# Performance work log

Measured on AMD Instinct MI355X. Metric: run time of the kernel, lower is better.

## Reference

```python
import jax, jax.numpy as jnp
import numpy as np

B, L, D, H, P = 4, 4096, 1024, 8, 4
DPH = D // H


def _grid_sample_row(v, grid):
    """F.grid_sample for a (N, C, 1, Lv) input, bilinear, padding_mode='zeros',
    align_corners=False. v: (N, C, Lv), grid: (N, Lq, P, 2) with (x, y) in last dim.
    Returns (N, C, Lq, P)."""
    N, C, Lv = v.shape
    x = grid[..., 0]
    y = grid[..., 1]
    # unnormalize (align_corners=False): u = ((coord + 1) * size - 1) / 2
    ux = ((x + 1.0) * Lv - 1.0) * 0.5          # width = Lv
    uy = ((y + 1.0) * 1.0 - 1.0) * 0.5         # height = 1
    x0f = jnp.floor(ux)
    wx1 = ux - x0f
    wx0 = 1.0 - wx1
    y0f = jnp.floor(uy)
    wy1 = uy - y0f
    wy0 = 1.0 - wy1
    # only row 0 exists; rows outside contribute zero (padding zeros)
    wy = wy0 * (y0f == 0.0) + wy1 * ((y0f + 1.0) == 0.0)   # (N, Lq, P)
    i0 = x0f.astype(jnp.int32)
    i1 = i0 + 1
    m0 = (i0 >= 0) & (i0 < Lv)
    m1 = (i1 >= 0) & (i1 < Lv)
    i0c = jnp.clip(i0, 0, Lv - 1)
    i1c = jnp.clip(i1, 0, Lv - 1)
    # gather along width per batch element: (C, Lv)[:, (Lq, P)] -> (C, Lq, P)
    v0 = jax.vmap(lambda vv, ii: vv[:, ii])(v, i0c)
    v1 = jax.vmap(lambda vv, ii: vv[:, ii])(v, i1c)
    w0 = (wx0 * m0 * wy)[:, None, :, :]
    w1 = (wx1 * m1 * wy)[:, None, :, :]
    return v0 * w0 + v1 * w1


def setup_inputs() -> dict:
    key = jax.random.key(0)
    ks = jax.random.split(key, 16)
    s = 0.02
    f32 = jnp.float32
    return {
        "query": jax.random.normal(ks[0], (B, L, D), f32),
        "key_in": jax.random.normal(ks[1], (B, L, D), f32),
        "value": jax.random.normal(ks[2], (B, L, D), f32),
        "Wqk": jax.random.normal(ks[3], (D, 2 * D), f32) * s,
        "bqk": jnp.zeros((2 * D,), f32),
        "Wv": jax.random.normal(ks[4], (D, D), f32) * s,
        "bv": jnp.zeros((D,), f32),
        "Woff": jax.random.normal(ks[5], (D, H * P * 2), f32) * s,
        "boff": jax.random.normal(ks[6], (H * P * 2,), f32) * 0.25,
        "Wattn": jax.random.normal(ks[7], (D, H * P), f32) * s,
        "battn": jnp.zeros((H * P,), f32),
        "Wo": jax.random.normal(ks[8], (D, D), f32) * s,
        "bo": jnp.zeros((D,), f32),
    }


def reference(query, key_in, value, Wqk, bqk, Wv, bv, Woff, boff, Wattn, battn, Wo, bo):
    # qk_proj: q, k are computed in the original but never used downstream (dead code)
    qk = query @ Wqk + bqk
    q, k = jnp.split(qk, 2, axis=-1)  # noqa: unused, matches original

    v = value @ Wv + bv                                   # (B, L, D)

    # reference points: x base = linspace[0] = 0, y base = i/(L-1) for query i
    ref_y = jnp.linspace(0.0, 1.0, L)
    ref = jnp.stack([jnp.zeros_like(ref_y), ref_y], axis=-1)   # (L, 2)

    offsets = (query @ Woff + boff).reshape(B, L, H, P, 2)
    attn = jax.nn.softmax((query @ Wattn + battn).reshape(B, L, H, P), axis=-1)

    loc = jnp.clip(ref[None, :, None, None, :] + offsets, 0.0, 1.0)  # (B, L, H, P, 2)

    # value -> (B*H, dph, L)
    vh = v.reshape(B, L, H, DPH).transpose(0, 2, 3, 1).reshape(B * H, DPH, L)
    grid = loc.transpose(0, 2, 1, 3, 4).reshape(B * H, L, P, 2)

    sampled = _grid_sample_row(vh, grid)                  # (B*H, dph, L, P)
    sampled = sampled.reshape(B, H, DPH, L, P)

    aw = attn.transpose(0, 2, 1, 3)[:, :, None, :, :]     # (B, H, 1, L, P)
    out = (sampled * aw).sum(-1)                          # (B, H, dph, L)
    out = out.transpose(0, 3, 1, 2).reshape(B, L, D)
    return out @ Wo + bo
```

## Files before the change

### kernel.cpp

```cpp
#include <hip/hip_runtime.h>

#define L_Q 4096
#define D_MODEL 1024
#define N_B 4
#define N_H 8
#define N_P 4
#define M_ROWS (N_B * L_Q)

typedef float f32x4 __attribute__((ext_vector_type(4)));
typedef __bf16 bf16x8 __attribute__((ext_vector_type(8)));
typedef unsigned short u16x8 __attribute__((ext_vector_type(8)));

__device__ __forceinline__ unsigned short f2bf(float f) {
    unsigned int u = __float_as_uint(f);
    u += 0x7FFFu + ((u >> 16) & 1u);
    return (unsigned short)(u >> 16);
}
__device__ __forceinline__ float bf2f(unsigned short s) {
    return __uint_as_float(((unsigned int)s) << 16);
}

__device__ __forceinline__ void gload_lds16(const void* g, void* l) {
    __builtin_amdgcn_global_load_lds((const __attribute__((address_space(1))) void*)g,
                                     (__attribute__((address_space(3))) void*)l,
                                     16, 0, 0);
}

template <int N> __device__ __forceinline__ void wait_vmc() {
    if constexpr (N == 6)      asm volatile("s_waitcnt vmcnt(6)"  ::: "memory");
    else if constexpr (N == 5) asm volatile("s_waitcnt vmcnt(5)"  ::: "memory");
    else if constexpr (N == 4) asm volatile("s_waitcnt vmcnt(4)"  ::: "memory");
    else                       asm volatile("s_waitcnt vmcnt(0)"  ::: "memory");
}


__global__ void k_cast_value(const float* __restrict__ in, unsigned short* __restrict__ out, int n4) {
    int i = blockIdx.x * blockDim.x + threadIdx.x;
    const int stride = gridDim.x * blockDim.x;
    for (; i < n4; i += stride) {
        float4 v = ((const float4*)in)[i];
        ushort4 o;
        o.x = f2bf(v.x); o.y = f2bf(v.y); o.z = f2bf(v.z); o.w = f2bf(v.w);
        ((ushort4*)out)[i] = o;
    }
}

__global__ void k_prep_weights(const float* __restrict__ Wv, const float* __restrict__ Wo,
                               const float* __restrict__ Woff, const float* __restrict__ Wattn,
                               unsigned short* __restrict__ WvT, unsigned short* __restrict__ WoT,
                               unsigned short* __restrict__ WcT2) {
    const int n1 = D_MODEL * D_MODEL;
    const int n2 = 2 * n1;
    const int n3 = n2 + 96 * 2048;
    int i = blockIdx.x * blockDim.x + threadIdx.x;
    const int stride = gridDim.x * blockDim.x;
    for (; i < n3; i += stride) {
        if (i < n1) {
            int n = i >> 10, k = i & 1023;
            WvT[i] = f2bf(Wv[k * D_MODEL + n]);
        } else if (i < n2) {
            int j = i - n1;
            int n = j >> 10, k = j & 1023;
            WoT[j] = f2bf(Wo[k * D_MODEL + n]);
        } else {
            int j = i - n2;
            int row = j >> 11;
            int rem = j & 2047;
            int half = rem >> 10;
            int k = rem & 1023;
            float w = (row < 64) ? Woff[k * 64 + row] : Wattn[k * 32 + (row - 64)];
            unsigned short h = f2bf(w);
            WcT2[j] = half ? f2bf(w - bf2f(h)) : h;
        }
    }
}


template <bool OUT_BF16>
__global__ __launch_bounds__(512, 2) void k_gemm256(const unsigned short* __restrict__ A,
                                                    const unsigned short* __restrict__ Bt,
                                                    const float* __restrict__ bias,
                                                    void* __restrict__ Cout) {
    __shared__ __align__(16) unsigned short lds[2][2][2][8192];
    const int tid = threadIdx.x;
    const int w = tid >> 6, lane = tid & 63;
    const int wm = w >> 2, wn = w & 3;

    const int bid = blockIdx.x;
    const int swz = (bid & 7) * 32 + (bid >> 3);
    const int m0 = (swz >> 2) * 256;
    const int n0 = (swz & 3) * 256;

    const int sr = (w << 3) + (lane >> 3);
    const int sc = (lane & 7) ^ ((lane >> 3) & 7);
    const size_t aoff1 = (size_t)(m0 + sr) * 1024 + (size_t)(sc * 8);
    const size_t boff1 = (size_t)(n0 + sr) * 1024 + (size_t)(sc * 8);

    const int fr = lane & 15, kq = lane >> 4;
    const int cs0 = ((kq) ^ (fr & 7)) * 8;
    const int cs1 = ((4 + kq) ^ (fr & 7)) * 8;
    const int arow = (wm * 64 + fr) * 64;
    const int brow = (wn * 32 + fr) * 64;

    f32x4 acc[2][2][4][2];
    const f32x4 zero = {0.f, 0.f, 0.f, 0.f};
#pragma unroll
    for (int qm = 0; qm < 2; ++qm)
#pragma unroll
        for (int qn = 0; qn < 2; ++qn)
#pragma unroll
            for (int i = 0; i < 4; ++i)
#pragma unroll
                for (int j = 0; j < 2; ++j) acc[qm][qn][i][j] = zero;

    bf16x8 af[4][2], bl[2][2], bh[2][2];

#define STAGE(mat, set, half, kt) do {                                                  \
        const unsigned short* g_ = ((mat) ? Bt : A) + ((mat) ? boff1 : aoff1)           \
                                   + (size_t)(half) * 131072 + (size_t)(kt);            \
        unsigned short* d_ = &lds[mat][set][half][0] + w * 512;                         \
        gload_lds16(g_, d_);                                                            \
        gload_lds16(g_ + 65536, d_ + 4096);                                             \
    } while (0)

#define LDA(set, qm) do {                                                               \
        const unsigned short* s_ = &lds[0][set][qm][0];                                 \
        _Pragma("unroll") for (int i = 0; i < 4; ++i) {                                 \
            af[i][0] = *(const bf16x8*)(s_ + arow + i * 1024 + cs0);                    \
            af[i][1] = *(const bf16x8*)(s_ + arow + i * 1024 + cs1);                    \
        }                                                                               \
    } while (0)

#define LDB(dst, set, qn) do {                                                          \
        const unsigned short* s_ = &lds[1][set][qn][0];                                 \
        _Pragma("unroll") for (int j = 0; j < 2; ++j) {                                 \
            dst[j][0] = *(const bf16x8*)(s_ + brow + j * 1024 + cs0);                   \
            dst[j][1] = *(const bf16x8*)(s_ + brow + j * 1024 + cs1);                   \
        }                                                                               \
    } while (0)

#define MM(qm, qn, B_) do {                                                             \
        __builtin_amdgcn_s_setprio(1);                                                  \
        _Pragma("unroll") for (int i = 0; i < 4; ++i)                                   \
        _Pragma("unroll") for (int j = 0; j < 2; ++j)                                   \
        _Pragma("unroll") for (int kk = 0; kk < 2; ++kk)                                \
            acc[qm][qn][i][j] = __builtin_amdgcn_mfma_f32_16x16x32_bf16(                \
                af[i][kk], B_[j][kk], acc[qm][qn][i][j], 0, 0, 0);                      \
        __builtin_amdgcn_s_setprio(0);                                                  \
    } while (0)

#define BAR() do { __builtin_amdgcn_s_barrier(); asm volatile("" ::: "memory"); } while (0)

    STAGE(0, 0, 0, 0);
    STAGE(1, 0, 0, 0);
    STAGE(1, 0, 1, 0);
    STAGE(0, 0, 1, 0);
    wait_vmc<4>();
    BAR();
    LDA(0, 0); LDB(bl, 0, 0);

#pragma unroll 1
    for (int it = 0; it < 8; ++it) {
        const int kt = it * 128;
        STAGE(0, 1, 0, kt + 64);
        wait_vmc<4>(); BAR();
        MM(0, 0, bl); LDB(bh, 0, 1);
        STAGE(1, 1, 0, kt + 64);
        wait_vmc<4>(); BAR();
        MM(0, 1, bh); LDA(0, 1);
        STAGE(1, 1, 1, kt + 64);
        wait_vmc<6>(); BAR();
        MM(1, 1, bh);
        STAGE(0, 1, 1, kt + 64);
        wait_vmc<4>(); BAR();
        MM(1, 0, bl); LDB(bl, 1, 0); LDA(1, 0);
        STAGE(0, 0, 0, kt + 128);
        wait_vmc<4>(); BAR();
        MM(0, 0, bl); LDB(bh, 1, 1);
        STAGE(1, 0, 0, kt + 128);
        wait_vmc<4>(); BAR();
        MM(0, 1, bh); LDA(1, 1);
        STAGE(1, 0, 1, kt + 128);
        wait_vmc<6>(); BAR();
        MM(1, 1, bh);
        STAGE(0, 0, 1, kt + 128);
        wait_vmc<4>(); BAR();
        MM(1, 0, bl); LDB(bl, 0, 0); LDA(0, 0);
    }
    wait_vmc<0>();

#undef STAGE
#undef LDA
#undef LDB
#undef MM
#undef BAR

#pragma unroll
    for (int qm = 0; qm < 2; ++qm) {
#pragma unroll
        for (int qn = 0; qn < 2; ++qn) {
#pragma unroll
            for (int i = 0; i < 4; ++i) {
#pragma unroll
                for (int j = 0; j < 2; ++j) {
                    const int col = n0 + qn * 128 + wn * 32 + j * 16 + fr;
                    const float bcol = bias[col];
#pragma unroll
                    for (int r = 0; r < 4; ++r) {
                        const int row = m0 + qm * 128 + wm * 64 + i * 16 + kq * 4 + r;
                        const float v = acc[qm][qn][i][j][r] + bcol;
                        if (OUT_BF16)
                            ((unsigned short*)Cout)[(size_t)row * D_MODEL + col] = f2bf(v);
                        else
                            ((float*)Cout)[(size_t)row * D_MODEL + col] = v;
                    }
                }
            }
        }
    }
}


__global__ __launch_bounds__(512, 2) void k_offattn2(const float* __restrict__ query,
                                                     const unsigned short* __restrict__ WcT2,
                                                     const float* __restrict__ boff,
                                                     const float* __restrict__ battn,
                                                     float* __restrict__ C96) {
    __shared__ __align__(16) unsigned short ldsA[2][128 * 64];
    __shared__ __align__(16) unsigned short ldsB[2][192 * 64];
    const int tid = threadIdx.x;
    const int w = tid >> 6, lane = tid & 63;
    const int wm = w >> 1, wn = w & 1;
    const int m0 = blockIdx.x * 64;

    const int ar = tid >> 3;
    const int ac = tid & 7;
    const float* qbase = query + (size_t)(m0 + ar) * 1024 + ac * 8;
    const int aw_hi = ar * 64 + ((ac ^ (ar & 7)) * 8);
    const int aw_lo = (64 + ar) * 64 + ((ac ^ (ar & 7)) * 8);

    const int brl = lane >> 3;
    const int bchk = (lane & 7) ^ (brl & 7);

    const int fr = lane & 15, kq = lane >> 4;
    const int cs0 = ((kq) ^ (fr & 7)) * 8;
    const int cs1 = ((4 + kq) ^ (fr & 7)) * 8;
    const int ahr = (wm * 16 + fr) * 64;
    const int alr = (64 + wm * 16 + fr) * 64;

    f32x4 acc[3];
    const f32x4 zero = {0.f, 0.f, 0.f, 0.f};
#pragma unroll
    for (int j = 0; j < 3; ++j) acc[j] = zero;

#define ALOAD(f0_, f1_, kt_) do {                                                       \
        f0_ = *(const float4*)(qbase + (kt_));                                          \
        f1_ = *(const float4*)(qbase + (kt_) + 4);                                      \
    } while (0)

#define BSTAGE(p_, kt_) do {                                                            \
        _Pragma("unroll") for (int i_ = 0; i_ < 3; ++i_) {                              \
            const int sr_ = i_ * 64 + w * 8 + brl;                                      \
            const unsigned short* g_ = WcT2 + ((sr_ < 96)                               \
                    ? ((size_t)sr_ * 2048 + (size_t)(kt_))                              \
                    : ((size_t)(sr_ - 96) * 2048 + 1024 + (size_t)(kt_)))               \
                    + (size_t)(bchk * 8);                                               \
            gload_lds16(g_, &ldsB[p_][(i_ * 64 + w * 8) * 64]);                         \
        }                                                                               \
    } while (0)

#define AWRITE(p_, f0_, f1_) do {                                                       \
        u16x8 hi_, lo_;                                                                 \
        const float vv_[8] = {f0_.x, f0_.y, f0_.z, f0_.w, f1_.x, f1_.y, f1_.z, f1_.w};  \
        _Pragma("unroll") for (int e_ = 0; e_ < 8; ++e_) {                              \
            hi_[e_] = f2bf(vv_[e_]);                                                    \
            lo_[e_] = f2bf(vv_[e_] - bf2f(hi_[e_]));                                    \
        }                                                                               \
        *(u16x8*)(&ldsA[p_][aw_hi]) = hi_;                                              \
        *(u16x8*)(&ldsA[p_][aw_lo]) = lo_;                                              \
    } while (0)

#define OMM(p_) do {                                                                    \
        const unsigned short* As_ = &ldsA[p_][0];                                       \
        const unsigned short* Bs_ = &ldsB[p_][0];                                       \
        bf16x8 ah0 = *(const bf16x8*)(As_ + ahr + cs0);                                 \
        bf16x8 ah1 = *(const bf16x8*)(As_ + ahr + cs1);                                 \
        bf16x8 al0 = *(const bf16x8*)(As_ + alr + cs0);                                 \
        bf16x8 al1 = *(const bf16x8*)(As_ + alr + cs1);                                 \
        __builtin_amdgcn_s_setprio(1);                                                  \
        _Pragma("unroll") for (int j = 0; j < 3; ++j) {                                 \
            const int br_ = (wn * 48 + j * 16 + fr) * 64;                               \
            bf16x8 wh0 = *(const bf16x8*)(Bs_ + br_ + cs0);                             \
            bf16x8 wh1 = *(const bf16x8*)(Bs_ + br_ + cs1);                             \
            bf16x8 wl0 = *(const bf16x8*)(Bs_ + 6144 + br_ + cs0);                      \
            bf16x8 wl1 = *(const bf16x8*)(Bs_ + 6144 + br_ + cs1);                      \
            acc[j] = __builtin_amdgcn_mfma_f32_16x16x32_bf16(ah0, wh0, acc[j], 0, 0, 0);\
            acc[j] = __builtin_amdgcn_mfma_f32_16x16x32_bf16(ah1, wh1, acc[j], 0, 0, 0);\
            acc[j] = __builtin_amdgcn_mfma_f32_16x16x32_bf16(ah0, wl0, acc[j], 0, 0, 0);\
            acc[j] = __builtin_amdgcn_mfma_f32_16x16x32_bf16(ah1, wl1, acc[j], 0, 0, 0);\
            acc[j] = __builtin_amdgcn_mfma_f32_16x16x32_bf16(al0, wh0, acc[j], 0, 0, 0);\
            acc[j] = __builtin_amdgcn_mfma_f32_16x16x32_bf16(al1, wh1, acc[j], 0, 0, 0);\
        }                                                                               \
        __builtin_amdgcn_s_setprio(0);                                                  \
    } while (0)

#define OBODY(t_, p_, fc0_, fc1_, fn0_, fn1_) do {                                      \
        if ((t_) < 15) {                                                                \
            ALOAD(fn0_, fn1_, ((t_) + 1) * 64);                                         \
            BSTAGE((p_) ^ 1, ((t_) + 1) * 64);                                          \
            wait_vmc<5>();                                                              \
        } else {                                                                        \
            wait_vmc<0>();                                                              \
        }                                                                               \
        AWRITE(p_, fc0_, fc1_);                                                         \
        asm volatile("s_waitcnt lgkmcnt(0)" ::: "memory");                              \
        __builtin_amdgcn_s_barrier(); asm volatile("" ::: "memory");                    \
        OMM(p_);                                                                        \
        __builtin_amdgcn_s_barrier(); asm volatile("" ::: "memory");                    \
    } while (0)

    float4 a0A, a1A, a0B, a1B;
    ALOAD(a0A, a1A, 0);
    BSTAGE(0, 0);

#pragma unroll 1
    for (int t2 = 0; t2 < 8; ++t2) {
        const int t = t2 * 2;
        OBODY(t,     0, a0A, a1A, a0B, a1B);
        OBODY(t + 1, 1, a0B, a1B, a0A, a1A);
    }

#undef ALOAD
#undef BSTAGE
#undef AWRITE
#undef OMM
#undef OBODY

#pragma unroll
    for (int j = 0; j < 3; ++j) {
        const int col = wn * 48 + j * 16 + fr;
        const float bcol = (col < 64) ? boff[col] : battn[col - 64];
#pragma unroll
        for (int r = 0; r < 4; ++r) {
            const int row = m0 + wm * 16 + kq * 4 + r;
            C96[(size_t)row * 96 + col] = acc[j][r] + bcol;
        }
    }
}


__global__ void k_sampler(const float* __restrict__ C96,
                          const unsigned short* __restrict__ vproj,
                          unsigned short* __restrict__ agg) {
    const int row = blockIdx.x;
    const int b = row >> 12;
    const int l = row & (L_Q - 1);
    const int t = threadIdx.x;

    __shared__ float cv[96];
    if (t < 96) cv[t] = C96[(size_t)row * 96 + t];
    __syncthreads();

    const int h = t >> 5;
    const int dd = (t & 31) * 4;
    const float ref_y = (float)l / 4095.0f;

    float lg[4];
#pragma unroll
    for (int p = 0; p < 4; ++p) lg[p] = cv[64 + h * 4 + p];
    const float mx = fmaxf(fmaxf(lg[0], lg[1]), fmaxf(lg[2], lg[3]));
    float ex[4];
    float es = 0.f;
#pragma unroll
    for (int p = 0; p < 4; ++p) { ex[p] = expf(lg[p] - mx); es += ex[p]; }
    const float inv = 1.0f / es;

    float acc0 = 0.f, acc1 = 0.f, acc2 = 0.f, acc3 = 0.f;
#pragma unroll
    for (int p = 0; p < 4; ++p) {
        const float ox = cv[h * 8 + p * 2];
        const float oy = cv[h * 8 + p * 2 + 1];
        const float lx = fminf(fmaxf(ox, 0.0f), 1.0f);
        const float ly = fminf(fmaxf(ref_y + oy, 0.0f), 1.0f);
        const float ux = (lx + 1.0f) * 2048.0f - 0.5f;
        const float wy = 1.0f - ly * 0.5f;
        const float x0f = floorf(ux);
        const int i0 = (int)x0f;
        const int i1 = i0 + 1;
        const float w1 = ux - x0f;
        const float w0 = 1.0f - w1;
        const float aw = ex[p] * inv * wy;
        const float f0 = aw * w0 * ((i0 >= 0 && i0 < L_Q) ? 1.0f : 0.0f);
        const float f1 = aw * w1 * ((i1 >= 0 && i1 < L_Q) ? 1.0f : 0.0f);
        const int i0c = i0 < 0 ? 0 : (i0 > L_Q - 1 ? L_Q - 1 : i0);
        const int i1c = i1 < 0 ? 0 : (i1 > L_Q - 1 ? L_Q - 1 : i1);
        const ushort4 v0 = *(const ushort4*)(vproj + (size_t)(b * L_Q + i0c) * D_MODEL + h * 128 + dd);
        const ushort4 v1 = *(const ushort4*)(vproj + (size_t)(b * L_Q + i1c) * D_MODEL + h * 128 + dd);
        acc0 += f0 * bf2f(v0.x) + f1 * bf2f(v1.x);
        acc1 += f0 * bf2f(v0.y) + f1 * bf2f(v1.y);
        acc2 += f0 * bf2f(v0.z) + f1 * bf2f(v1.z);
        acc3 += f0 * bf2f(v0.w) + f1 * bf2f(v1.w);
    }
    ushort4 o;
    o.x = f2bf(acc0); o.y = f2bf(acc1); o.z = f2bf(acc2); o.w = f2bf(acc3);
    *(ushort4*)(agg + (size_t)row * D_MODEL + t * 4) = o;
}


extern "C" void kernel_launch(void* const* d_in, const int* in_sizes, int n_in,
                              void* d_out, int out_size, void* d_ws, size_t ws_size,
                              hipStream_t stream) {
    const float* query = (const float*)d_in[0];
    const float* value = (const float*)d_in[2];
    const float* Wv    = (const float*)d_in[5];
    const float* bv    = (const float*)d_in[6];
    const float* Woff  = (const float*)d_in[7];
    const float* boff  = (const float*)d_in[8];
    const float* Wattn = (const float*)d_in[9];
    const float* battn = (const float*)d_in[10];
    const float* Wo    = (const float*)d_in[11];
    const float* bo    = (const float*)d_in[12];

    char* ws = (char*)d_ws;
    size_t off = 0;
    auto alloc = [&](size_t bytes) -> char* {
        char* p = ws + off;
        off += (bytes + 255) & ~(size_t)255;
        return p;
    };
    unsigned short* val_bf = (unsigned short*)alloc((size_t)M_ROWS * D_MODEL * 2);
    unsigned short* vproj  = (unsigned short*)alloc((size_t)M_ROWS * D_MODEL * 2);
    unsigned short* agg    = (unsigned short*)alloc((size_t)M_ROWS * D_MODEL * 2);
    float*          C96    = (float*)alloc((size_t)M_ROWS * 96 * 4);
    unsigned short* WvT    = (unsigned short*)alloc((size_t)D_MODEL * D_MODEL * 2);
    unsigned short* WoT    = (unsigned short*)alloc((size_t)D_MODEL * D_MODEL * 2);
    unsigned short* WcT2   = (unsigned short*)alloc((size_t)96 * 2048 * 2);

    const int n4 = M_ROWS * D_MODEL / 4;
    k_cast_value<<<2048, 256, 0, stream>>>(value, val_bf, n4);
    k_prep_weights<<<1024, 256, 0, stream>>>(Wv, Wo, Woff, Wattn, WvT, WoT, WcT2);

    k_gemm256<true><<<256, 512, 0, stream>>>(val_bf, WvT, bv, vproj);

    k_offattn2<<<M_ROWS / 64, 512, 0, stream>>>(query, WcT2, boff, battn, C96);

    k_sampler<<<M_ROWS, 256, 0, stream>>>(C96, vproj, agg);

    k_gemm256<false><<<256, 512, 0, stream>>>(agg, WoT, bo, (float*)d_out);
}
```

Baseline: 152.6 us.

## Fuse fp32-to-bf16 value cast into value-projection GEMM A-tile loading

Removes the standalone value cast kernel and its bf16 intermediate buffer. The value GEMM now reads fp32 A tiles through registers, converts them to bf16 and writes them into swizzled LDS, all interleaved with the existing MFMA pipeline. This avoids one full write and re-read of the 16M-element value tensor plus a kernel launch. In exchange the GEMM reads twice as many A bytes, uses more VGPRs for the prefetch registers, and the pipeline now contains register-staged writes with extra waits that could stall MFMA issue.

Measured after the change: 152.2 us. No clear change (-0.2%).

```diff
diff --git a/kernel.cpp b/kernel.cpp
--- a/kernel.cpp
+++ b/kernel.cpp
@@ -19,6 +19,12 @@
 __device__ __forceinline__ float bf2f(unsigned short s) {
     return __uint_as_float(((unsigned int)s) << 16);
 }
+__device__ __forceinline__ u16x8 cvt8(float4 a, float4 b) {
+    u16x8 r;
+    r[0] = f2bf(a.x); r[1] = f2bf(a.y); r[2] = f2bf(a.z); r[3] = f2bf(a.w);
+    r[4] = f2bf(b.x); r[5] = f2bf(b.y); r[6] = f2bf(b.z); r[7] = f2bf(b.w);
+    return r;
+}
 
 __device__ __forceinline__ void gload_lds16(const void* g, void* l) {
     __builtin_amdgcn_global_load_lds((const __attribute__((address_space(1))) void*)g,
@@ -33,17 +39,6 @@
     else                       asm volatile("s_waitcnt vmcnt(0)"  ::: "memory");
 }
 
-
-__global__ void k_cast_value(const float* __restrict__ in, unsigned short* __restrict__ out, int n4) {
-    int i = blockIdx.x * blockDim.x + threadIdx.x;
-    const int stride = gridDim.x * blockDim.x;
-    for (; i < n4; i += stride) {
-        float4 v = ((const float4*)in)[i];
-        ushort4 o;
-        o.x = f2bf(v.x); o.y = f2bf(v.y); o.z = f2bf(v.z); o.w = f2bf(v.w);
-        ((ushort4*)out)[i] = o;
-    }
-}
 
 __global__ void k_prep_weights(const float* __restrict__ Wv, const float* __restrict__ Wo,
                                const float* __restrict__ Woff, const float* __restrict__ Wattn,
@@ -76,8 +71,8 @@
 }
 
 
-template <bool OUT_BF16>
-__global__ __launch_bounds__(512, 2) void k_gemm256(const unsigned short* __restrict__ A,
+template <bool A_F32, bool OUT_BF16>
+__global__ __launch_bounds__(512, 2) void k_gemm256(const void* __restrict__ Ain,
                                                     const unsigned short* __restrict__ Bt,
                                                     const float* __restrict__ bias,
                                                     void* __restrict__ Cout) {
@@ -95,6 +90,14 @@
     const int sc = (lane & 7) ^ ((lane >> 3) & 7);
     const size_t aoff1 = (size_t)(m0 + sr) * 1024 + (size_t)(sc * 8);
     const size_t boff1 = (size_t)(n0 + sr) * 1024 + (size_t)(sc * 8);
+    const unsigned short* Ab = (const unsigned short*)Ain;
+
+    const int frow = tid >> 2;
+    const int fcol = (tid & 3) * 16;
+    const float* fA = (const float*)Ain + (size_t)(m0 + frow) * 1024 + fcol;
+    const int fc0 = fcol >> 3;
+    const int awr0 = frow * 64 + ((fc0 ^ (frow & 7)) * 8);
+    const int awr1 = frow * 64 + (((fc0 + 1) ^ (frow & 7)) * 8);
 
     const int fr = lane & 15, kq = lane >> 4;
     const int cs0 = ((kq) ^ (fr & 7)) * 8;
@@ -114,13 +117,34 @@
                 for (int j = 0; j < 2; ++j) acc[qm][qn][i][j] = zero;
 
     bf16x8 af[4][2], bl[2][2], bh[2][2];
-
-#define STAGE(mat, set, half, kt) do {                                                  \
-        const unsigned short* g_ = ((mat) ? Bt : A) + ((mat) ? boff1 : aoff1)           \
-                                   + (size_t)(half) * 131072 + (size_t)(kt);            \
-        unsigned short* d_ = &lds[mat][set][half][0] + w * 512;                         \
+    float4 pA0, pA1, pA2, pA3, pB0, pB1, pB2, pB3;
+
+#define GSTA(set, half, kt) do {                                                        \
+        const unsigned short* g_ = Ab + aoff1 + (size_t)(half) * 131072 + (size_t)(kt); \
+        unsigned short* d_ = &lds[0][set][half][0] + w * 512;                           \
         gload_lds16(g_, d_);                                                            \
         gload_lds16(g_ + 65536, d_ + 4096);                                             \
+    } while (0)
+
+#define GSTB(set, half, kt) do {                                                        \
+        const unsigned short* g_ = Bt + boff1 + (size_t)(half) * 131072 + (size_t)(kt); \
+        unsigned short* d_ = &lds[1][set][half][0] + w * 512;                           \
+        gload_lds16(g_, d_);                                                            \
+        gload_lds16(g_ + 65536, d_ + 4096);                                             \
+    } while (0)
+
+#define AISSUE(P_, half, kt) do {                                                       \
+        const float* s_ = fA + (size_t)(half) * 131072 + (size_t)(kt);                  \
+        P_##0 = *(const float4*)(s_);                                                   \
+        P_##1 = *(const float4*)(s_ + 4);                                               \
+        P_##2 = *(const float4*)(s_ + 8);                                               \
+        P_##3 = *(const float4*)(s_ + 12);                                              \
+    } while (0)
+
+#define AWRITE(P_, set, half) do {                                                      \
+        *(u16x8*)(&lds[0][set][half][awr0]) = cvt8(P_##0, P_##1);                       \
+        *(u16x8*)(&lds[0][set][half][awr1]) = cvt8(P_##2, P_##3);                       \
+        asm volatile("s_waitcnt lgkmcnt(0)" ::: "memory");                              \
     } while (0)
 
 #define LDA(set, qm) do {                                                               \
@@ -151,45 +175,87 @@
 
 #define BAR() do { __builtin_amdgcn_s_barrier(); asm volatile("" ::: "memory"); } while (0)
 
-    STAGE(0, 0, 0, 0);
-    STAGE(1, 0, 0, 0);
-    STAGE(1, 0, 1, 0);
-    STAGE(0, 0, 1, 0);
-    wait_vmc<4>();
-    BAR();
+    if constexpr (A_F32) {
+        AISSUE(pA, 0, 0);
+        GSTB(0, 0, 0);
+        GSTB(0, 1, 0);
+        wait_vmc<4>();
+        AWRITE(pA, 0, 0);
+        AISSUE(pB, 1, 0);
+        wait_vmc<6>();
+        BAR();
+    } else {
+        GSTA(0, 0, 0);
+        GSTB(0, 0, 0);
+        GSTB(0, 1, 0);
+        GSTA(0, 1, 0);
+        wait_vmc<4>();
+        BAR();
+    }
     LDA(0, 0); LDB(bl, 0, 0);
 
 #pragma unroll 1
     for (int it = 0; it < 8; ++it) {
         const int kt = it * 128;
-        STAGE(0, 1, 0, kt + 64);
-        wait_vmc<4>(); BAR();
-        MM(0, 0, bl); LDB(bh, 0, 1);
-        STAGE(1, 1, 0, kt + 64);
-        wait_vmc<4>(); BAR();
-        MM(0, 1, bh); LDA(0, 1);
-        STAGE(1, 1, 1, kt + 64);
-        wait_vmc<6>(); BAR();
-        MM(1, 1, bh);
-        STAGE(0, 1, 1, kt + 64);
-        wait_vmc<4>(); BAR();
-        MM(1, 0, bl); LDB(bl, 1, 0); LDA(1, 0);
-        STAGE(0, 0, 0, kt + 128);
-        wait_vmc<4>(); BAR();
-        MM(0, 0, bl); LDB(bh, 1, 1);
-        STAGE(1, 0, 0, kt + 128);
-        wait_vmc<4>(); BAR();
-        MM(0, 1, bh); LDA(1, 1);
-        STAGE(1, 0, 1, kt + 128);
-        wait_vmc<6>(); BAR();
-        MM(1, 1, bh);
-        STAGE(0, 0, 1, kt + 128);
-        wait_vmc<4>(); BAR();
-        MM(1, 0, bl); LDB(bl, 0, 0); LDA(0, 0);
+        const int ktn = (kt + 128) & 1023;
+        if constexpr (A_F32) {
+            AISSUE(pA, 0, kt + 64);
+            wait_vmc<4>(); AWRITE(pB, 0, 1); BAR();
+            MM(0, 0, bl); LDB(bh, 0, 1);
+            GSTB(1, 0, kt + 64);
+            BAR();
+            MM(0, 1, bh); LDA(0, 1);
+            GSTB(1, 1, kt + 64);
+            wait_vmc<4>(); AWRITE(pA, 1, 0); BAR();
+            MM(1, 1, bh);
+            AISSUE(pB, 1, kt + 64);
+            wait_vmc<6>(); BAR();
+            MM(1, 0, bl); LDB(bl, 1, 0); LDA(1, 0);
+            AISSUE(pA, 0, ktn);
+            wait_vmc<4>(); AWRITE(pB, 1, 1); BAR();
+            MM(0, 0, bl); LDB(bh, 1, 1);
+            GSTB(0, 0, ktn);
+            BAR();
+            MM(0, 1, bh); LDA(1, 1);
+            GSTB(0, 1, ktn);
+            wait_vmc<4>(); AWRITE(pA, 0, 0); BAR();
+            MM(1, 1, bh);
+            AISSUE(pB, 1, ktn);
+            wait_vmc<6>(); BAR();
+            MM(1, 0, bl); LDB(bl, 0, 0); LDA(0, 0);
+        } else {
+            GSTA(1, 0, kt + 64);
+            wait_vmc<4>(); BAR();
+            MM(0, 0, bl); LDB(bh, 0, 1);
+            GSTB(1, 0, kt + 64);
+            wait_vmc<4>(); BAR();
+            MM(0, 1, bh); LDA(0, 1);
+            GSTB(1, 1, kt + 64);
+            wait_vmc<6>(); BAR();
+            MM(1, 1, bh);
+            GSTA(1, 1, kt + 64);
+            wait_vmc<4>(); BAR();
+            MM(1, 0, bl); LDB(bl, 1, 0); LDA(1, 0);
+            GSTA(0, 0, ktn);
+            wait_vmc<4>(); BAR();
+            MM(0, 0, bl); LDB(bh, 1, 1);
+            GSTB(0, 0, ktn);
+            wait_vmc<4>(); BAR();
+            MM(0, 1, bh); LDA(1, 1);
+            GSTB(0, 1, ktn);
+            wait_vmc<6>(); BAR();
+            MM(1, 1, bh);
+            GSTA(0, 1, ktn);
+            wait_vmc<4>(); BAR();
+            MM(1, 0, bl); LDB(bl, 0, 0); LDA(0, 0);
+        }
     }
     wait_vmc<0>();
 
-#undef STAGE
+#undef GSTA
+#undef GSTB
+#undef AISSUE
+#undef AWRITE
 #undef LDA
 #undef LDB
 #undef MM
@@ -269,7 +335,7 @@
         }                                                                               \
     } while (0)
 
-#define AWRITE(p_, f0_, f1_) do {                                                       \
+#define AWRITE2(p_, f0_, f1_) do {                                                      \
         u16x8 hi_, lo_;                                                                 \
         const float vv_[8] = {f0_.x, f0_.y, f0_.z, f0_.w, f1_.x, f1_.y, f1_.z, f1_.w};  \
         _Pragma("unroll") for (int e_ = 0; e_ < 8; ++e_) {                              \
@@ -312,7 +378,7 @@
         } else {                                                                        \
             wait_vmc<0>();                                                              \
         }                                                                               \
-        AWRITE(p_, fc0_, fc1_);                                                         \
+        AWRITE2(p_, fc0_, fc1_);                                                        \
         asm volatile("s_waitcnt lgkmcnt(0)" ::: "memory");                              \
         __builtin_amdgcn_s_barrier(); asm volatile("" ::: "memory");                    \
         OMM(p_);                                                                        \
@@ -332,7 +398,7 @@
 
 #undef ALOAD
 #undef BSTAGE
-#undef AWRITE
+#undef AWRITE2
 #undef OMM
 #undef OBODY
 
@@ -428,7 +494,6 @@
         off += (bytes + 255) & ~(size_t)255;
         return p;
     };
-    unsigned short* val_bf = (unsigned short*)alloc((size_t)M_ROWS * D_MODEL * 2);
     unsigned short* vproj  = (unsigned short*)alloc((size_t)M_ROWS * D_MODEL * 2);
     unsigned short* agg    = (unsigned short*)alloc((size_t)M_ROWS * D_MODEL * 2);
     float*          C96    = (float*)alloc((size_t)M_ROWS * 96 * 4);
@@ -436,15 +501,13 @@
     unsigned short* WoT    = (unsigned short*)alloc((size_t)D_MODEL * D_MODEL * 2);
     unsigned short* WcT2   = (unsigned short*)alloc((size_t)96 * 2048 * 2);
 
-    const int n4 = M_ROWS * D_MODEL / 4;
-    k_cast_value<<<2048, 256, 0, stream>>>(value, val_bf, n4);
     k_prep_weights<<<1024, 256, 0, stream>>>(Wv, Wo, Woff, Wattn, WvT, WoT, WcT2);
 
-    k_gemm256<true><<<256, 512, 0, stream>>>(val_bf, WvT, bv, vproj);
+    k_gemm256<true, true><<<256, 512, 0, stream>>>(value, WvT, bv, vproj);
 
     k_offattn2<<<M_ROWS / 64, 512, 0, stream>>>(query, WcT2, boff, battn, C96);
 
     k_sampler<<<M_ROWS, 256, 0, stream>>>(C96, vproj, agg);
 
-    k_gemm256<false><<<256, 512, 0, stream>>>(agg, WoT, bo, (float*)d_out);
-}
+    k_gemm256<false, false><<<256, 512, 0, stream>>>(agg, WoT, bo, (float*)d_out);
+}
```
